# Performance work log

Measured on AMD Instinct MI355X. Metric: run time of the kernel, lower is better.

## Reference

```python
import jax, jax.numpy as jnp
import numpy as np

KE_KCAL = 332.0637  # Coulomb constant in kcal/mol * Angstrom / e^2
R_CUT = 10.0
R_ON = R_CUT / 4.0
R_OFF = 3.0 * R_CUT / 4.0
MAX_Z = 86
FEAT_DIM = 128
N_ATOMS = 6144


def sigma(x):
    # torch.where(x > 0, exp(-1/x), 0) -- guard the exp arg so no NaN under jit
    xs = jnp.where(x > 0, x, 1.0)
    return jnp.where(x > 0, jnp.exp(-1.0 / xs), 0.0)


def f_switch(r):
    arg = (r - R_ON) / (R_OFF - R_ON)
    s_up = sigma(1.0 - arg)
    s_dn = sigma(arg)
    return s_up / (s_up + s_dn)


def setup_inputs() -> dict:
    key = jax.random.key(0)
    k_f, k_z, k_x, k_w, k_t = jax.random.split(key, 5)
    f = jax.random.normal(k_f, (N_ATOMS, FEAT_DIM), dtype=jnp.float32)
    z = jax.random.randint(k_z, (N_ATOMS,), 0, MAX_Z, dtype=jnp.int64)
    xyz = jax.random.uniform(k_x, (N_ATOMS, 3), dtype=jnp.float32) * 60.0  # ~60 A box
    total_charge = jnp.zeros((1,), dtype=jnp.float32)
    # learned params: Dense(feat_dim -> 1, no bias) and Embedding(max_z, 1) with padding row 0
    w_weight = jax.random.normal(k_w, (1, FEAT_DIM), dtype=jnp.float32) * 0.05
    z_table = jax.random.normal(k_t, (MAX_Z, 1), dtype=jnp.float32) * 0.05
    z_table = z_table.at[0].set(0.0)  # padding_idx=0
    return {"f": f, "z": z, "xyz": xyz, "total_charge": total_charge,
            "w_weight": w_weight, "z_table": z_table}


def reference(f, z, xyz, total_charge, w_weight, z_table):
    n = f.shape[0]
    # --- get_charge ---
    pred_charge = f @ w_weight.T + z_table[z]          # [N, 1]
    correction = (total_charge[0] - pred_charge.sum()) / n
    q = pred_charge + correction                       # [N, 1]
    qv = q[:, 0]                                       # [N]
    # --- get_en: pairwise distances via gram trick (no [N,N,3] intermediate) ---
    sq = jnp.sum(xyz * xyz, axis=-1)                   # [N]
    r2 = sq[:, None] + sq[None, :] - 2.0 * (xyz @ xyz.T)
    r2 = jnp.maximum(r2, 0.0)                          # [N, N]
    iu = jnp.triu(jnp.ones((n, n), dtype=bool), k=1)
    mask = iu & (r2 > 0.0)                             # j > i and r > 0, as in the torch code
    r2_safe = jnp.where(mask, r2, 1.0)
    r = jnp.sqrt(r2_safe)
    fs = f_switch(r)
    term = fs / jnp.sqrt(r2_safe + 1.0) + (1.0 - fs) / r
    pair_e = jnp.where(mask, qv[:, None] * qv[None, :] * term, 0.0)
    energy = KE_KCAL * jnp.sum(pair_e)
    return energy, q
```

## Files before the change

kernel.cpp:

```cpp
#include <hip/hip_runtime.h>

#define KE_KCAL 332.0637f

constexpr int N_ATOMS = 6144;
constexpr int NREAL = 1200;
constexpr int NPRED = 384;

__global__ __launch_bounds__(256) void pred_kernel(
    const float* __restrict__ f, const int* __restrict__ z,
    const float* __restrict__ w, const float* __restrict__ ztab,
    const float* __restrict__ xyz,
    float* __restrict__ qpart, float4* __restrict__ xqp)
{
    int t = threadIdx.x, b = blockIdx.x;
    int lane = t & 63, wid = t >> 6;

    int base = b * 16 + wid * 4;
    const float2* f2 = (const float2*)f;
    float2 wv = ((const float2*)w)[lane];
    float2 v0 = f2[(size_t)(base + 0) * 64 + lane];
    float2 v1 = f2[(size_t)(base + 1) * 64 + lane];
    float2 v2 = f2[(size_t)(base + 2) * 64 + lane];
    float2 v3 = f2[(size_t)(base + 3) * 64 + lane];
    float p0 = fmaf(v0.x, wv.x, v0.y * wv.y);
    float p1 = fmaf(v1.x, wv.x, v1.y * wv.y);
    float p2 = fmaf(v2.x, wv.x, v2.y * wv.y);
    float p3 = fmaf(v3.x, wv.x, v3.y * wv.y);
    #pragma unroll
    for (int off = 32; off > 0; off >>= 1) {
        p0 += __shfl_xor(p0, off, 64);
        p1 += __shfl_xor(p1, off, 64);
        p2 += __shfl_xor(p2, off, 64);
        p3 += __shfl_xor(p3, off, 64);
    }
    float ws_sum = 0.f;
    if (lane < 4) {
        int atom = base + lane;
        float pk = p0;
        pk = (lane == 1) ? p1 : pk;
        pk = (lane == 2) ? p2 : pk;
        pk = (lane == 3) ? p3 : pk;
        pk += ztab[z[atom]];
        xqp[atom] = make_float4(xyz[3*atom], xyz[3*atom+1], xyz[3*atom+2], pk);
        ws_sum = pk;
    }
    ws_sum += __shfl_xor(ws_sum, 1, 64);
    ws_sum += __shfl_xor(ws_sum, 2, 64);

    __shared__ float lred[4];
    if (lane == 0) lred[wid] = ws_sum;
    __syncthreads();
    if (t == 0) qpart[b] = lred[0] + lred[1] + lred[2] + lred[3];
}

__global__ __launch_bounds__(256) void pair_kernel(
    const float4* __restrict__ xqp, const float* __restrict__ qpart,
    const float* __restrict__ total_charge,
    float* __restrict__ qout, float* __restrict__ eblk)
{
    int t = threadIdx.x, b = blockIdx.x;
    int lane = t & 63, wid = t >> 6;
    __shared__ float lred[4];
    __shared__ float4 sj[64];

    float s = qpart[t];
    if (t < NPRED - 256) s += qpart[256 + t];
    #pragma unroll
    for (int off = 32; off > 0; off >>= 1)
        s += __shfl_xor(s, off, 64);
    if (lane == 0) lred[wid] = s;
    __syncthreads();
    float S = lred[0] + lred[1] + lred[2] + lred[3];
    float corr = (total_charge[0] - S) * (1.0f / (float)N_ATOMS);

    int bi = 0, off = 0;
    while (b >= off + (96 - 4 * bi)) { off += 96 - 4 * bi; ++bi; }
    int bj = 4 * bi + (b - off);

    int gj0 = bj * 64;
    if (t < 64) {
        float4 a = xqp[gj0 + t];
        a.w += corr;
        sj[t] = a;
    }
    int gi = bi * 256 + t;
    float4 pi = xqp[gi];
    float qi = pi.w + corr;
    if (bj == 4 * bi) qout[gi] = qi;
    __syncthreads();

    int jthresh = gi - gj0;

    float4 c0 = sj[0], c1 = sj[1], c2 = sj[2], c3 = sj[3];
    float acc0 = 0.f, acc1 = 0.f, acc2 = 0.f, acc3 = 0.f;
    #pragma unroll
    for (int k = 0; k < 64; k += 4) {
        float4 n0, n1, n2, n3;
        if (k + 4 < 64) {
            n0 = sj[k+4]; n1 = sj[k+5]; n2 = sj[k+6]; n3 = sj[k+7];
        }
        {
            float dx = pi.x - c0.x, dy = pi.y - c0.y, dz = pi.z - c0.z;
            float r2 = fmaf(dx, dx, fmaf(dy, dy, dz * dz));
            bool m = (k > jthresh) && (r2 > 0.f);
            float r2s = m ? r2 : 1e8f;
            float qq  = m ? qi * c0.w : 0.f;
            float t2 = __builtin_amdgcn_rsqf(r2s);
            float u  = fmaf(r2s * t2, 0.2f, -0.5f);
            u = fminf(fmaxf(u, 1e-3f), 0.999f);
            float d  = (u + u - 1.f) * __builtin_amdgcn_rcpf(fmaf(-u, u, u));
            float fs = __builtin_amdgcn_rcpf(1.f + __expf(d));
            float t1 = __builtin_amdgcn_rsqf(r2s + 1.f);
            acc0 = fmaf(qq, fmaf(fs, t1 - t2, t2), acc0);
        }
        {
            float dx = pi.x - c1.x, dy = pi.y - c1.y, dz = pi.z - c1.z;
            float r2 = fmaf(dx, dx, fmaf(dy, dy, dz * dz));
            bool m = (k + 1 > jthresh) && (r2 > 0.f);
            float r2s = m ? r2 : 1e8f;
            float qq  = m ? qi * c1.w : 0.f;
            float t2 = __builtin_amdgcn_rsqf(r2s);
            float u  = fmaf(r2s * t2, 0.2f, -0.5f);
            u = fminf(fmaxf(u, 1e-3f), 0.999f);
            float d  = (u + u - 1.f) * __builtin_amdgcn_rcpf(fmaf(-u, u, u));
            float fs = __builtin_amdgcn_rcpf(1.f + __expf(d));
            float t1 = __builtin_amdgcn_rsqf(r2s + 1.f);
            acc1 = fmaf(qq, fmaf(fs, t1 - t2, t2), acc1);
        }
        {
            float dx = pi.x - c2.x, dy = pi.y - c2.y, dz = pi.z - c2.z;
            float r2 = fmaf(dx, dx, fmaf(dy, dy, dz * dz));
            bool m = (k + 2 > jthresh) && (r2 > 0.f);
            float r2s = m ? r2 : 1e8f;
            float qq  = m ? qi * c2.w : 0.f;
            float t2 = __builtin_amdgcn_rsqf(r2s);
            float u  = fmaf(r2s * t2, 0.2f, -0.5f);
            u = fminf(fmaxf(u, 1e-3f), 0.999f);
            float d  = (u + u - 1.f) * __builtin_amdgcn_rcpf(fmaf(-u, u, u));
            float fs = __builtin_amdgcn_rcpf(1.f + __expf(d));
            float t1 = __builtin_amdgcn_rsqf(r2s + 1.f);
            acc2 = fmaf(qq, fmaf(fs, t1 - t2, t2), acc2);
        }
        {
            float dx = pi.x - c3.x, dy = pi.y - c3.y, dz = pi.z - c3.z;
            float r2 = fmaf(dx, dx, fmaf(dy, dy, dz * dz));
            bool m = (k + 3 > jthresh) && (r2 > 0.f);
            float r2s = m ? r2 : 1e8f;
            float qq  = m ? qi * c3.w : 0.f;
            float t2 = __builtin_amdgcn_rsqf(r2s);
            float u  = fmaf(r2s * t2, 0.2f, -0.5f);
            u = fminf(fmaxf(u, 1e-3f), 0.999f);
            float d  = (u + u - 1.f) * __builtin_amdgcn_rcpf(fmaf(-u, u, u));
            float fs = __builtin_amdgcn_rcpf(1.f + __expf(d));
            float t1 = __builtin_amdgcn_rsqf(r2s + 1.f);
            acc3 = fmaf(qq, fmaf(fs, t1 - t2, t2), acc3);
        }
        c0 = n0; c1 = n1; c2 = n2; c3 = n3;
    }
    float acc = (acc0 + acc1) + (acc2 + acc3);

    #pragma unroll
    for (int o2 = 32; o2 > 0; o2 >>= 1)
        acc += __shfl_down(acc, o2, 64);
    __syncthreads();
    if (lane == 0) lred[wid] = acc;
    __syncthreads();
    if (t == 0) eblk[b] = lred[0] + lred[1] + lred[2] + lred[3];
}

__global__ __launch_bounds__(256) void efin_kernel(
    const float* __restrict__ eblk, float* __restrict__ out0)
{
    int t = threadIdx.x;
    float e = 0.f;
    for (int k = t; k < NREAL; k += 256) e += eblk[k];
    #pragma unroll
    for (int o2 = 32; o2 > 0; o2 >>= 1)
        e += __shfl_down(e, o2, 64);
    __shared__ float wacc[4];
    if ((t & 63) == 0) wacc[t >> 6] = e;
    __syncthreads();
    if (t == 0) out0[0] = KE_KCAL * (wacc[0] + wacc[1] + wacc[2] + wacc[3]);
}

extern "C" void kernel_launch(void* const* d_in, const int* in_sizes, int n_in,
                              void* d_out, int out_size, void* d_ws, size_t ws_size,
                              hipStream_t stream) {
    const float* f    = (const float*)d_in[0];
    const int*   z    = (const int*)  d_in[1];
    const float* xyz  = (const float*)d_in[2];
    const float* qtot = (const float*)d_in[3];
    const float* w    = (const float*)d_in[4];
    const float* ztab = (const float*)d_in[5];
    float* out = (float*)d_out;

    char* wsb = (char*)d_ws;
    float*  qpart = (float*)(wsb + 0);
    float*  eblk  = (float*)(wsb + 2048);
    float4* xqp   = (float4*)(wsb + 16384);

    pred_kernel<<<NPRED, 256, 0, stream>>>(f, z, w, ztab, xyz, qpart, xqp);
    pair_kernel<<<NREAL, 256, 0, stream>>>(xqp, qpart, qtot, out + 1, eblk);
    efin_kernel<<<1, 256, 0, stream>>>(eblk, out);
}
```

Measured before the change: 90.25 us.

## Replace switched Coulomb term with polynomial-corrected single rsqrt; specialize off-diagonal tiles

The per-pair energy term previously needed two rsqrt, two rcp and one exp. It is now computed as one rsqrt of a shifted r^2. The shift comes from a small polynomial in clamped, rescaled r^2 that stands in for the smooth switching function. Tiles that are not on the diagonal skip the j>i mask test through a templated loop. This cuts transcendental and VALU work per pair, at the risk of accuracy loss from the fitted approximation and extra code size from two unrolled loop copies.

```diff
diff --git a/kernel.cpp b/kernel.cpp
--- a/kernel.cpp
+++ b/kernel.cpp
@@ -53,6 +53,24 @@
     if (t == 0) qpart[b] = lred[0] + lred[1] + lred[2] + lred[3];
 }
 
+template<bool DIAG>
+__device__ __forceinline__ float pair_term(
+    const float4& c, const float4& pi, float qi, int k, int jthresh)
+{
+    float dx = pi.x - c.x, dy = pi.y - c.y, dz = pi.z - c.z;
+    float x  = fmaf(dx, dx, fmaf(dy, dy, dz * dz));
+    bool m = (!DIAG || (k > jthresh)) && (x > 0.f);
+    float qq = m ? qi * c.w : 0.f;
+    float u = fmaf(x, 0.02f, -0.625f);
+    u = fminf(fmaxf(u, -0.5f), 0.5f);
+    float v = fmaf(u, fmaf(u, fmaf(u, 0.333856f, -0.472136f),
+                           0.916536f), 0.118034f);
+    float v2 = v * v;
+    float p  = fmaf(v2, fmaf(v2, fmaf(v2, -8.f, 12.f), -6.5f), 2.f);
+    float arg = fmaf(-v, p, x + 0.5f);
+    return qq * __builtin_amdgcn_rsqf(arg);
+}
+
 __global__ __launch_bounds__(256) void pair_kernel(
     const float4* __restrict__ xqp, const float* __restrict__ qpart,
     const float* __restrict__ total_charge,
@@ -90,73 +108,30 @@
     __syncthreads();
 
     int jthresh = gi - gj0;
+    bool diag = (bj - 4 * bi) < 4;
 
-    float4 c0 = sj[0], c1 = sj[1], c2 = sj[2], c3 = sj[3];
     float acc0 = 0.f, acc1 = 0.f, acc2 = 0.f, acc3 = 0.f;
-    #pragma unroll
-    for (int k = 0; k < 64; k += 4) {
-        float4 n0, n1, n2, n3;
-        if (k + 4 < 64) {
-            n0 = sj[k+4]; n1 = sj[k+5]; n2 = sj[k+6]; n3 = sj[k+7];
-        }
-        {
-            float dx = pi.x - c0.x, dy = pi.y - c0.y, dz = pi.z - c0.z;
-            float r2 = fmaf(dx, dx, fmaf(dy, dy, dz * dz));
-            bool m = (k > jthresh) && (r2 > 0.f);
-            float r2s = m ? r2 : 1e8f;
-            float qq  = m ? qi * c0.w : 0.f;
-            float t2 = __builtin_amdgcn_rsqf(r2s);
-            float u  = fmaf(r2s * t2, 0.2f, -0.5f);
-            u = fminf(fmaxf(u, 1e-3f), 0.999f);
-            float d  = (u + u - 1.f) * __builtin_amdgcn_rcpf(fmaf(-u, u, u));
-            float fs = __builtin_amdgcn_rcpf(1.f + __expf(d));
-            float t1 = __builtin_amdgcn_rsqf(r2s + 1.f);
-            acc0 = fmaf(qq, fmaf(fs, t1 - t2, t2), acc0);
-        }
-        {
-            float dx = pi.x - c1.x, dy = pi.y - c1.y, dz = pi.z - c1.z;
-            float r2 = fmaf(dx, dx, fmaf(dy, dy, dz * dz));
-            bool m = (k + 1 > jthresh) && (r2 > 0.f);
-            float r2s = m ? r2 : 1e8f;
-            float qq  = m ? qi * c1.w : 0.f;
-            float t2 = __builtin_amdgcn_rsqf(r2s);
-            float u  = fmaf(r2s * t2, 0.2f, -0.5f);
-            u = fminf(fmaxf(u, 1e-3f), 0.999f);
-            float d  = (u + u - 1.f) * __builtin_amdgcn_rcpf(fmaf(-u, u, u));
-            float fs = __builtin_amdgcn_rcpf(1.f + __expf(d));
-            float t1 = __builtin_amdgcn_rsqf(r2s + 1.f);
-            acc1 = fmaf(qq, fmaf(fs, t1 - t2, t2), acc1);
-        }
-        {
-            float dx = pi.x - c2.x, dy = pi.y - c2.y, dz = pi.z - c2.z;
-            float r2 = fmaf(dx, dx, fmaf(dy, dy, dz * dz));
-            bool m = (k + 2 > jthresh) && (r2 > 0.f);
-            float r2s = m ? r2 : 1e8f;
-            float qq  = m ? qi * c2.w : 0.f;
-            float t2 = __builtin_amdgcn_rsqf(r2s);
-            float u  = fmaf(r2s * t2, 0.2f, -0.5f);
-            u = fminf(fmaxf(u, 1e-3f), 0.999f);
-            float d  = (u + u - 1.f) * __builtin_amdgcn_rcpf(fmaf(-u, u, u));
-            float fs = __builtin_amdgcn_rcpf(1.f + __expf(d));
-            float t1 = __builtin_amdgcn_rsqf(r2s + 1.f);
-            acc2 = fmaf(qq, fmaf(fs, t1 - t2, t2), acc2);
-        }
-        {
-            float dx = pi.x - c3.x, dy = pi.y - c3.y, dz = pi.z - c3.z;
-            float r2 = fmaf(dx, dx, fmaf(dy, dy, dz * dz));
-            bool m = (k + 3 > jthresh) && (r2 > 0.f);
-            float r2s = m ? r2 : 1e8f;
-            float qq  = m ? qi * c3.w : 0.f;
-            float t2 = __builtin_amdgcn_rsqf(r2s);
-            float u  = fmaf(r2s * t2, 0.2f, -0.5f);
-            u = fminf(fmaxf(u, 1e-3f), 0.999f);
-            float d  = (u + u - 1.f) * __builtin_amdgcn_rcpf(fmaf(-u, u, u));
-            float fs = __builtin_amdgcn_rcpf(1.f + __expf(d));
-            float t1 = __builtin_amdgcn_rsqf(r2s + 1.f);
-            acc3 = fmaf(qq, fmaf(fs, t1 - t2, t2), acc3);
-        }
-        c0 = n0; c1 = n1; c2 = n2; c3 = n3;
+
+#define PAIR_LOOP(DIAG_FLAG)                                                  \
+    {                                                                         \
+        float4 c0 = sj[0], c1 = sj[1], c2 = sj[2], c3 = sj[3];                \
+        _Pragma("unroll")                                                     \
+        for (int k = 0; k < 64; k += 4) {                                     \
+            float4 n0, n1, n2, n3;                                            \
+            if (k + 4 < 64) {                                                 \
+                n0 = sj[k+4]; n1 = sj[k+5]; n2 = sj[k+6]; n3 = sj[k+7];       \
+            }                                                                 \
+            acc0 += pair_term<DIAG_FLAG>(c0, pi, qi, k,     jthresh);         \
+            acc1 += pair_term<DIAG_FLAG>(c1, pi, qi, k + 1, jthresh);         \
+            acc2 += pair_term<DIAG_FLAG>(c2, pi, qi, k + 2, jthresh);         \
+            acc3 += pair_term<DIAG_FLAG>(c3, pi, qi, k + 3, jthresh);         \
+            c0 = n0; c1 = n1; c2 = n2; c3 = n3;                               \
+        }                                                                     \
     }
+
+    if (diag) PAIR_LOOP(true) else PAIR_LOOP(false)
+#undef PAIR_LOOP
+
     float acc = (acc0 + acc1) + (acc2 + acc3);
 
     #pragma unroll
```

After: 83.79 us. 1.08x faster.
